# Performance work log

Hardware: AMD Instinct MI355X
Metric: run time of the kernel (lower is better)

The kernel has to match this reference:

```python
import jax, jax.numpy as jnp
import numpy as np

N = 50000      # num_nodes
E = 800000     # num_edges
D = 128        # hidden_dim
POOL_RATIO = 0.5
CROSS_W = 1.0  # cross_weight


def _gcn(x, W, b, src, dst, n):
    """GCNConv: symmetric-normalized aggregation with self-loops. Dropout is identity (eval)."""
    loops = jnp.arange(n)
    s = jnp.concatenate([src, loops])
    d = jnp.concatenate([dst, loops])
    deg = jax.ops.segment_sum(jnp.ones(s.shape, x.dtype), d, num_segments=n)
    inv_sqrt = jax.lax.rsqrt(jnp.maximum(deg, 1.0))  # deg >= 1 due to self-loops
    xw = x @ W                                        # [n, D]
    msg = xw[s] * (inv_sqrt[s] * inv_sqrt[d])[:, None]  # [E+n, D] gather
    return jax.ops.segment_sum(msg, d, num_segments=n) + b


def _prelu(x, a):
    return jnp.where(x >= 0, x, a * x)


def setup_inputs() -> dict:
    key = jax.random.key(0)
    ks = jax.random.split(key, 8)
    glorot = lambda k, sh: jax.random.normal(k, sh, jnp.float32) * np.float32(np.sqrt(2.0 / (sh[0] + sh[1])))
    return {
        "feat": jax.random.normal(ks[0], (N, D), jnp.float32),
        "h_neg": jax.random.normal(ks[1], (N, D), jnp.float32),
        "edge_index": jax.random.randint(ks[2], (2, E), 0, N),
        "Wd": glorot(ks[3], (D, D)),
        "bd": jnp.zeros((D,), jnp.float32),
        "prelu_a": jnp.full((1,), 0.25, jnp.float32),
        "Wbil": glorot(ks[4], (D, D)),
        "bbil": jnp.zeros((1,), jnp.float32),
        "Wg1": glorot(ks[5], (D, D)),
        "bg1": jnp.zeros((D,), jnp.float32),
        "Wg2": glorot(ks[6], (D, D)),
        "bg2": jnp.zeros((D,), jnp.float32),
        "Wg3": glorot(ks[7], (D, D)),
        "bg3": jnp.zeros((D,), jnp.float32),
    }


def reference(feat, h_neg, edge_index, Wd, bd, prelu_a, Wbil, bbil,
              Wg1, bg1, Wg2, bg2, Wg3, bg3):
    src, dst = edge_index[0], edge_index[1]
    # --- IndexSelect: dense layer on pos/neg features ---
    h_pos = _prelu(feat @ Wd + bd, prelu_a)
    h_neg_d = _prelu(h_neg @ Wd + bd, prelu_a)
    embed = _gcn(h_pos, Wg1, bg1, src, dst, N)
    h_center = jax.nn.sigmoid(embed)
    # Discriminator (bilinear) positive scores -> node importance
    score_pos = jnp.einsum('nd,de,ne->n', h_pos, Wbil, h_center) + bbil[0]
    _ = jnp.einsum('nd,de,ne->n', h_neg_d, Wbil, h_center) + bbil[0]  # score_neg (logits branch)
    scores = jax.nn.sigmoid(score_pos)
    order = jnp.argsort(-scores)           # descending
    k = int(POOL_RATIO * N)
    select_idx = order[:k]
    select_scores = scores[order][:k]
    # --- GraphPool (use_gcn=True): down-sample GCN, gather, scale ---
    pooled = _gcn(embed, Wg2, bg2, src, dst, N)[select_idx] * select_scores[:, None]
    # --- GraphUnpool: scatter into zeros, up-sample GCN ---
    fine = jnp.zeros((N, D), feat.dtype).at[select_idx].set(pooled)
    out = _gcn(fine, Wg3, bg3, src, dst, N)
    # --- cross/fuse connection ---
    return out + CROSS_W * embed
```

## Files before the change

kernel.cpp:

```cpp
#include <hip/hip_runtime.h>
#include <hip/hip_bf16.h>

#define NN 50000
#define NE 800000
#define DD 128
#define KSEL 25000
#define NBK 391
#define NBLKA 98

typedef unsigned int uint32;
typedef unsigned short ushort16;

__device__ __forceinline__ float sigmoidf(float x){ return 1.f/(1.f+__expf(-x)); }

__device__ __forceinline__ unsigned short f2b(float f){
  union{float f; unsigned u;} v; v.f=f;
  unsigned r=(v.u + 0x7fffu + ((v.u>>16)&1u))>>16;
  return (unsigned short)r;
}

__device__ __forceinline__ void addbf2(float&lo,float&hi,uint32 u,float w){
  lo+=__uint_as_float(u<<16)*w;
  hi+=__uint_as_float(u&0xffff0000u)*w;
}

__global__ __launch_bounds__(1024) void k_bcount(const int* __restrict__ dst,
    int* __restrict__ btot, int* __restrict__ blkcnt){
  __shared__ int h[NBK];
  int tid=threadIdx.x;
  for(int i=tid;i<NBK;i+=1024) h[i]=0;
  __syncthreads();
  int e0=blockIdx.x*8192;
  #pragma unroll
  for(int t=0;t<8;t++){
    int e=e0+t*1024+tid;
    if(e<NE) atomicAdd(&h[dst[e]>>7],1);
  }
  __syncthreads();
  for(int i=tid;i<NBK;i+=1024){
    int c=h[i];
    blkcnt[blockIdx.x*NBK+i]=c;
    if(c) atomicAdd(&btot[i],c);
  }
}

__global__ __launch_bounds__(512) void k_bscan(const int* __restrict__ btot,
    int* __restrict__ boff, const int* __restrict__ blkcnt, int* __restrict__ blkbase,
    int* __restrict__ row_start){
  __shared__ int sdata[512];
  int tid=threadIdx.x;
  int v=(tid<NBK)?btot[tid]:0;
  sdata[tid]=v; __syncthreads();
  for(int off=1;off<512;off<<=1){
    int y=(tid>=off)?sdata[tid-off]:0;
    __syncthreads();
    sdata[tid]+=y;
    __syncthreads();
  }
  int excl=sdata[tid]-v;
  if(tid<NBK) boff[tid]=excl;
  if(tid==NBK-1){ boff[NBK]=excl+v; row_start[NN]=NE; }
  if(tid<NBK){
    int run=excl;
    for(int b=0;b<NBLKA;b++){
      int c=blkcnt[b*NBK+tid];
      blkbase[b*NBK+tid]=run;
      run+=c;
    }
  }
}

__global__ __launch_bounds__(1024) void k_bscatter(const int* __restrict__ src,
    const int* __restrict__ dst, const int* __restrict__ blkbase, uint32* __restrict__ pairs){
  __shared__ int cur[NBK];
  int tid=threadIdx.x;
  for(int i=tid;i<NBK;i+=1024) cur[i]=blkbase[blockIdx.x*NBK+i];
  __syncthreads();
  int e0=blockIdx.x*8192;
  #pragma unroll
  for(int t=0;t<8;t++){
    int e=e0+t*1024+tid;
    if(e<NE){
      int d=dst[e];
      int p=atomicAdd(&cur[d>>7],1);
      pairs[p]=(unsigned)src[e] | ((unsigned)(d&127)<<17);
    }
  }
}

__global__ __launch_bounds__(256) void k_bfinal(const uint32* __restrict__ pairs,
    const int* __restrict__ boff, int* __restrict__ row_start,
    float* __restrict__ inv_sq, int* __restrict__ csr_src){
  __shared__ int degl[128];
  __shared__ int cur[128];
  __shared__ int ssum[2];
  int b=blockIdx.x, tid=threadIdx.x;
  int lo=boff[b], hi=boff[b+1];
  if(tid<128) degl[tid]=0;
  __syncthreads();
  for(int e=lo+tid;e<hi;e+=256) atomicAdd(&degl[pairs[e]>>17],1);
  __syncthreads();
  int v=0,x=0;
  if(tid<128){
    v=degl[tid]; x=v;
    #pragma unroll
    for(int off=1;off<64;off<<=1){
      int y=__shfl_up(x,off,64);
      if((tid&63)>=off) x+=y;
    }
    if((tid&63)==63) ssum[tid>>6]=x;
  }
  __syncthreads();
  if(tid<128){
    int incl=x+((tid>=64)?ssum[0]:0);
    int node=b*128+tid;
    int excl=lo+incl-v;
    if(node<NN){
      row_start[node]=excl;
      cur[tid]=excl;
      inv_sq[node]=1.f/sqrtf((float)(v+1));
    }
  }
  __syncthreads();
  for(int e=lo+tid;e<hi;e+=256){
    uint32 u=pairs[e];
    int p=atomicAdd(&cur[u>>17],1);
    csr_src[p]=(int)(u&0x1FFFFu);
  }
}

__global__ void k_transpose(const float* __restrict__ W, float* __restrict__ Wt){
  int idx=blockIdx.x*256+threadIdx.x;
  if(idx<DD*DD){
    int k=idx>>7, c=idx&127;
    Wt[idx]=W[c*DD+k];
  }
}

template<int IN_SIG,int ACT,int OUT_BF16,int FUSE_SCORE,int ROWLIST>
__global__ __launch_bounds__(256) void k_gemm96(const float* __restrict__ A,
    const float* __restrict__ W, const float* __restrict__ bias,
    float* __restrict__ outf, ushort16* __restrict__ outb,
    const float* __restrict__ aparam, const float* __restrict__ hp,
    const float* __restrict__ bbil, float* __restrict__ score,
    const int* __restrict__ rlist){
  __shared__ float Al[96][132];
  int tid=threadIdx.x;
  int row0=blockIdx.x*96;
  {
    #pragma unroll
    for(int i=0;i<12;i++){
      int idx=i*256+tid;
      int r=idx>>5, c=(idx&31)*4;
      int gr; bool ok;
      if(ROWLIST){ int ri=row0+r; ok=(ri<KSEL); gr=ok?rlist[ri]:0; }
      else { gr=row0+r; ok=(gr<NN); }
      float4 v=make_float4(0.f,0.f,0.f,0.f);
      if(ok) v=*(const float4*)&A[(size_t)gr*DD+c];
      if(IN_SIG){ v.x=sigmoidf(v.x); v.y=sigmoidf(v.y); v.z=sigmoidf(v.z); v.w=sigmoidf(v.w); }
      *(float4*)&Al[r][c]=v;
    }
  }
  __syncthreads();
  int tx=tid&15, ty=tid>>4;
  float acc[6][8];
  #pragma unroll
  for(int i=0;i<6;i++)
    #pragma unroll
    for(int c=0;c<8;c++) acc[i][c]=0.f;

  for(int k=0;k<DD;k+=4){
    float wv[4][8];
    #pragma unroll
    for(int r=0;r<4;r++){
      float4 lo=*(const float4*)&W[(size_t)(k+r)*DD+tx*8];
      float4 hi=*(const float4*)&W[(size_t)(k+r)*DD+tx*8+4];
      wv[r][0]=lo.x; wv[r][1]=lo.y; wv[r][2]=lo.z; wv[r][3]=lo.w;
      wv[r][4]=hi.x; wv[r][5]=hi.y; wv[r][6]=hi.z; wv[r][7]=hi.w;
    }
    #pragma unroll
    for(int i=0;i<6;i++){
      float4 a=*(const float4*)&Al[ty+16*i][k];
      #pragma unroll
      for(int c=0;c<8;c++)
        acc[i][c]+=a.x*wv[0][c]+a.y*wv[1][c]+a.z*wv[2][c]+a.w*wv[3][c];
    }
  }

  if(FUSE_SCORE){
    float bb=bbil[0];
    #pragma unroll
    for(int i=0;i<6;i++){
      int r=row0+ty+16*i;
      float p=0.f;
      if(r<NN){
        float4 h0=*(const float4*)&hp[(size_t)r*DD+tx*8];
        float4 h1=*(const float4*)&hp[(size_t)r*DD+tx*8+4];
        p=acc[i][0]*h0.x+acc[i][1]*h0.y+acc[i][2]*h0.z+acc[i][3]*h0.w
         +acc[i][4]*h1.x+acc[i][5]*h1.y+acc[i][6]*h1.z+acc[i][7]*h1.w;
      }
      p+=__shfl_xor(p,1,64); p+=__shfl_xor(p,2,64);
      p+=__shfl_xor(p,4,64); p+=__shfl_xor(p,8,64);
      if(tx==0 && r<NN) score[r]=sigmoidf(p+bb);
    }
    return;
  }
  float bl[8]={0,0,0,0,0,0,0,0};
  if(bias){
    float4 b0=*(const float4*)&bias[tx*8];
    float4 b1=*(const float4*)&bias[tx*8+4];
    bl[0]=b0.x; bl[1]=b0.y; bl[2]=b0.z; bl[3]=b0.w;
    bl[4]=b1.x; bl[5]=b1.y; bl[6]=b1.z; bl[7]=b1.w;
  }
  float ap=ACT?aparam[0]:0.f;
  #pragma unroll
  for(int i=0;i<6;i++){
    int ri=row0+ty+16*i;
    int r; bool ok;
    if(ROWLIST){ ok=(ri<KSEL); r=ok?rlist[ri]:0; }
    else { r=ri; ok=(r<NN); }
    if(ok){
      float o[8];
      #pragma unroll
      for(int c=0;c<8;c++){
        float t=acc[i][c]+bl[c];
        if(ACT) t=t>=0.f?t:ap*t;
        o[c]=t;
      }
      if(OUT_BF16){
        uint4 pk;
        pk.x=((uint32)f2b(o[1])<<16)|f2b(o[0]);
        pk.y=((uint32)f2b(o[3])<<16)|f2b(o[2]);
        pk.z=((uint32)f2b(o[5])<<16)|f2b(o[4]);
        pk.w=((uint32)f2b(o[7])<<16)|f2b(o[6]);
        *(uint4*)&outb[(size_t)r*DD+tx*8]=pk;
      } else {
        float4 q0; q0.x=o[0]; q0.y=o[1]; q0.z=o[2]; q0.w=o[3];
        float4 q1; q1.x=o[4]; q1.y=o[5]; q1.z=o[6]; q1.w=o[7];
        *(float4*)&outf[(size_t)r*DD+tx*8]=q0;
        *(float4*)&outf[(size_t)r*DD+tx*8+4]=q1;
      }
    }
  }
}

__global__ __launch_bounds__(256) void k_agg_f32(const float* __restrict__ xw,
    const int* __restrict__ row_start, const int* __restrict__ csr,
    const float* __restrict__ inv, const float* __restrict__ bias,
    float* __restrict__ outp){
  int node=blockIdx.x*4+(threadIdx.x>>6);
  if(node>=NN) return;
  int lane=threadIdx.x&63;
  int g=lane>>5, li=lane&31;
  int rs=row_start[node], re=row_start[node+1];
  float a0=0.f,a1=0.f,a2=0.f,a3=0.f;
  int j=rs;
  for(; j+7<re; j+=8){
    int s0=csr[j+g], s1=csr[j+2+g], s2=csr[j+4+g], s3=csr[j+6+g];
    float w0=inv[s0], w1=inv[s1], w2=inv[s2], w3=inv[s3];
    float4 v0=*(const float4*)&xw[(size_t)s0*DD+li*4];
    float4 v1=*(const float4*)&xw[(size_t)s1*DD+li*4];
    float4 v2=*(const float4*)&xw[(size_t)s2*DD+li*4];
    float4 v3=*(const float4*)&xw[(size_t)s3*DD+li*4];
    a0+=v0.x*w0+v1.x*w1+v2.x*w2+v3.x*w3;
    a1+=v0.y*w0+v1.y*w1+v2.y*w2+v3.y*w3;
    a2+=v0.z*w0+v1.z*w1+v2.z*w2+v3.z*w3;
    a3+=v0.w*w0+v1.w*w1+v2.w*w2+v3.w*w3;
  }
  for(; j+1<re; j+=2){
    int s=csr[j+g];
    float w=inv[s];
    float4 v=*(const float4*)&xw[(size_t)s*DD+li*4];
    a0+=v.x*w; a1+=v.y*w; a2+=v.z*w; a3+=v.w*w;
  }
  if(j<re && g==0){
    int s=csr[j]; float w=inv[s];
    float4 v=*(const float4*)&xw[(size_t)s*DD+li*4];
    a0+=v.x*w; a1+=v.y*w; a2+=v.z*w; a3+=v.w*w;
  }
  if(g==0){
    float wd=inv[node];
    float4 v=*(const float4*)&xw[(size_t)node*DD+li*4];
    a0+=v.x*wd; a1+=v.y*wd; a2+=v.z*wd; a3+=v.w*wd;
  }
  a0+=__shfl_xor(a0,32,64); a1+=__shfl_xor(a1,32,64);
  a2+=__shfl_xor(a2,32,64); a3+=__shfl_xor(a3,32,64);
  if(g==0){
    float wn=inv[node];
    float4 bv=*(const float4*)&bias[li*4];
    float4 o;
    o.x=a0*wn+bv.x; o.y=a1*wn+bv.y; o.z=a2*wn+bv.z; o.w=a3*wn+bv.w;
    *(float4*)&outp[(size_t)node*DD+li*4]=o;
  }
}

template<int MODE>
__global__ __launch_bounds__(256) void k_agg_b16(const uint32* __restrict__ xwb,
    const int* __restrict__ row_start, const int* __restrict__ csr,
    const float* __restrict__ inv, const float* __restrict__ bias,
    float* __restrict__ outp, const float* __restrict__ score,
    const unsigned char* __restrict__ sel, const float* __restrict__ addbuf,
    const int* __restrict__ list){
  int idx4=blockIdx.x*4+(threadIdx.x>>6);
  int node;
  if(MODE==1){ if(idx4>=KSEL) return; node=list[idx4]; }
  else { node=idx4; if(node>=NN) return; }
  int lane=threadIdx.x&63;
  int g=lane>>4, li=lane&15;
  int rs=row_start[node], re=row_start[node+1];
  float a[8];
  #pragma unroll
  for(int c=0;c<8;c++) a[c]=0.f;
  int j=rs;
  for(; j+7<re; j+=8){
    int sA=csr[j+g], sB=csr[j+4+g];
    if(MODE!=2 || sel[sA]){
      float w=inv[sA];
      uint4 u=*(const uint4*)(xwb+(size_t)sA*64+li*4);
      addbf2(a[0],a[1],u.x,w); addbf2(a[2],a[3],u.y,w);
      addbf2(a[4],a[5],u.z,w); addbf2(a[6],a[7],u.w,w);
    }
    if(MODE!=2 || sel[sB]){
      float w=inv[sB];
      uint4 u=*(const uint4*)(xwb+(size_t)sB*64+li*4);
      addbf2(a[0],a[1],u.x,w); addbf2(a[2],a[3],u.y,w);
      addbf2(a[4],a[5],u.z,w); addbf2(a[6],a[7],u.w,w);
    }
  }
  for(; j+3<re; j+=4){
    int s=csr[j+g];
    if(MODE!=2 || sel[s]){
      float w=inv[s];
      uint4 u=*(const uint4*)(xwb+(size_t)s*64+li*4);
      addbf2(a[0],a[1],u.x,w); addbf2(a[2],a[3],u.y,w);
      addbf2(a[4],a[5],u.z,w); addbf2(a[6],a[7],u.w,w);
    }
  }
  int rem=re-j;
  if(g<rem){
    int s=csr[j+g];
    if(MODE!=2 || sel[s]){
      float w=inv[s];
      uint4 u=*(const uint4*)(xwb+(size_t)s*64+li*4);
      addbf2(a[0],a[1],u.x,w); addbf2(a[2],a[3],u.y,w);
      addbf2(a[4],a[5],u.z,w); addbf2(a[6],a[7],u.w,w);
    }
  }
  if(g==0 && (MODE!=2 || sel[node])){
    float wd=inv[node];
    uint4 u=*(const uint4*)(xwb+(size_t)node*64+li*4);
    addbf2(a[0],a[1],u.x,wd); addbf2(a[2],a[3],u.y,wd);
    addbf2(a[4],a[5],u.z,wd); addbf2(a[6],a[7],u.w,wd);
  }
  #pragma unroll
  for(int c=0;c<8;c++){
    a[c]+=__shfl_xor(a[c],16,64);
    a[c]+=__shfl_xor(a[c],32,64);
  }
  if(g<2){
    float wn=inv[node];
    int cb=li*8+g*4;
    float4 bv=*(const float4*)&bias[cb];
    float r0=a[g*4+0]*wn+bv.x, r1=a[g*4+1]*wn+bv.y;
    float r2=a[g*4+2]*wn+bv.z, r3=a[g*4+3]*wn+bv.w;
    if(MODE==1){
      float sc=score[node];
      r0*=sc; r1*=sc; r2*=sc; r3*=sc;
    } else {
      float4 ad=*(const float4*)&addbuf[(size_t)node*DD+cb];
      r0+=ad.x; r1+=ad.y; r2+=ad.z; r3+=ad.w;
    }
    float4 o; o.x=r0; o.y=r1; o.z=r2; o.w=r3;
    *(float4*)&outp[(size_t)node*DD+cb]=o;
  }
}

template<int NB,int PASS>
__global__ __launch_bounds__(256) void k_hist(const float* __restrict__ score,
    int* __restrict__ ghist, const int* __restrict__ ctrl){
  __shared__ int lh[NB];
  int tid=threadIdx.x;
  for(int i=tid;i<NB;i+=256) lh[i]=0;
  __syncthreads();
  int p0=0,p01=0;
  if(PASS==1) p0=ctrl[0];
  if(PASS==2) p01=ctrl[2];
  for(int i=blockIdx.x*256+tid; i<NN; i+=gridDim.x*256){
    unsigned b=__float_as_uint(score[i]);
    if(PASS==0) atomicAdd(&lh[b>>20],1);
    else if(PASS==1){ if((int)(b>>20)==p0) atomicAdd(&lh[(b>>8)&0xFFF],1); }
    else { if((int)(b>>8)==p01) atomicAdd(&lh[b&0xFF],1); }
  }
  __syncthreads();
  for(int i=tid;i<NB;i+=256){ int v=lh[i]; if(v) atomicAdd(&ghist[i],v); }
}

template<int NB,int PASS>
__global__ void k_findb(const int* __restrict__ hist, int* __restrict__ ctrl){
  const int NT=NB/4;
  __shared__ int gsum[NT];
  int t=threadIdx.x;
  int s=hist[t*4]+hist[t*4+1]+hist[t*4+2]+hist[t*4+3];
  int x=s; gsum[t]=x; __syncthreads();
  for(int off=1;off<NT;off<<=1){
    int y=(t+off<NT)?gsum[t+off]:0;
    __syncthreads();
    x+=y; gsum[t]=x; __syncthreads();
  }
  int base;
  if(PASS==0) base=0; else if(PASS==1) base=ctrl[1]; else base=ctrl[3];
  int above=base+((t<NT-1)?gsum[t+1]:0);
  int incl=base+gsum[t];
  if(above<KSEL && incl>=KSEL){
    int c=above, B=0;
    for(int b=3;b>=0;b--){
      int hb=hist[t*4+b];
      if(c+hb>=KSEL){ B=t*4+b; break; }
      c+=hb;
    }
    if(PASS==0){ ctrl[0]=B; ctrl[1]=c; }
    else if(PASS==1){ ctrl[2]=(ctrl[0]<<12)|B; ctrl[3]=c; }
    else { ctrl[4]=(int)((((unsigned)ctrl[2])<<8)|(unsigned)B); ctrl[5]=KSEL-c; }
  }
}

__global__ void k_sel(const float* __restrict__ score, int* __restrict__ ctrl,
                      int* __restrict__ tie_list, unsigned char* __restrict__ sel,
                      int* __restrict__ list){
  int i=blockIdx.x*256+threadIdx.x;
  if(i>=NN) return;
  unsigned b=__float_as_uint(score[i]);
  unsigned thr=(unsigned)ctrl[4];
  if(b>thr){
    sel[i]=1;
    int p=atomicAdd(&ctrl[7],1);
    list[p]=i;
  }
  else if(b==thr){
    sel[i]=0;
    int p=atomicAdd(&ctrl[6],1);
    if(p<4096) tie_list[p]=i;
  } else sel[i]=0;
}

__global__ __launch_bounds__(256) void k_tie(const int* __restrict__ ctrl_c,
    int* __restrict__ ctrl, const int* __restrict__ tie_list,
    unsigned char* __restrict__ sel, int* __restrict__ list){
  int m=ctrl_c[6]; if(m>4096) m=4096;
  int needed=ctrl_c[5];
  for(int t=threadIdx.x; t<m; t+=blockDim.x){
    int idx=tie_list[t];
    int rank=0;
    for(int j=0;j<m;j++) rank+=(tie_list[j]<idx)?1:0;
    if(rank<needed){
      sel[idx]=1;
      int p=atomicAdd(&ctrl[7],1);
      list[p]=idx;
    }
  }
}

extern "C" void kernel_launch(void* const* d_in, const int* in_sizes, int n_in,
                              void* d_out, int out_size, void* d_ws, size_t ws_size,
                              hipStream_t stream){
  const float* feat   =(const float*)d_in[0];
  const int*   ei     =(const int*)  d_in[2];
  const int*   src    = ei;
  const int*   dst    = ei + NE;
  const float* Wd     =(const float*)d_in[3];
  const float* bd     =(const float*)d_in[4];
  const float* prelu_a=(const float*)d_in[5];
  const float* Wbil   =(const float*)d_in[6];
  const float* bbil   =(const float*)d_in[7];
  const float* Wg1    =(const float*)d_in[8];
  const float* bg1    =(const float*)d_in[9];
  const float* Wg2    =(const float*)d_in[10];
  const float* bg2    =(const float*)d_in[11];
  const float* Wg3    =(const float*)d_in[12];
  const float* bg3    =(const float*)d_in[13];
  float* out=(float*)d_out;

  char* p=(char*)d_ws;
  auto alloc=[&](size_t bytes)->void*{ void* r=(void*)p; p+=((bytes+255)/256)*256; return r; };
  float* h_pos   =(float*)alloc((size_t)NN*DD*4);
  float* embed   =(float*)alloc((size_t)NN*DD*4);
  float* xw      =(float*)alloc((size_t)NN*DD*4);
  float* score   =(float*)alloc((size_t)NN*4);
  float* inv_sq  =(float*)alloc((size_t)NN*4);
  float* WbT     =(float*)alloc((size_t)DD*DD*4);
  int*   row_st  =(int*)  alloc((size_t)(NN+1)*4);
  int*   csr_src =(int*)  alloc((size_t)NE*4);
  int*   ctrl    =(int*)  alloc(64);
  int*   hist0   =(int*)  alloc(4096*4);
  int*   hist1   =(int*)  alloc(4096*4);
  int*   hist2   =(int*)  alloc(256*4);
  int*   tie_list=(int*)  alloc(4096*4);
  int*   list    =(int*)  alloc((size_t)KSEL*4);
  unsigned char* sel=(unsigned char*)alloc(NN);
  int*   btot    =(int*)  alloc((size_t)NBK*4);
  int*   boff    =(int*)  alloc((size_t)(NBK+1)*4);
  int*   blkcnt  =(int*)  alloc((size_t)NBLKA*NBK*4);
  int*   blkbase =(int*)  alloc((size_t)NBLKA*NBK*4);
  uint32* pairs  =(uint32*)xw;
  ushort16* xwb  =(ushort16*)xw;
  float* fine = out;

  const int NB=(NN+255)/256;
  const int GB=(NN+95)/96;
  const int GBL=(KSEL+95)/96;
  const int AB=(NN+3)/4;
  const int ABL=(KSEL+3)/4;

  hipMemsetAsync(ctrl, 0, (size_t)((char*)tie_list-(char*)ctrl), stream);
  hipMemsetAsync(btot, 0, (size_t)NBK*4, stream);

  k_bcount  <<<NBLKA,1024,0,stream>>>(dst, btot, blkcnt);
  k_bscan   <<<1,512,0,stream>>>(btot, boff, blkcnt, blkbase, row_st);
  k_bscatter<<<NBLKA,1024,0,stream>>>(src, dst, blkbase, pairs);
  k_bfinal  <<<NBK,256,0,stream>>>(pairs, boff, row_st, inv_sq, csr_src);
  k_transpose<<<64,256,0,stream>>>(Wbil, WbT);

  k_gemm96<0,1,0,0,0><<<GB,256,0,stream>>>(feat, Wd, bd, h_pos, nullptr, prelu_a, nullptr, nullptr, nullptr, nullptr);
  k_gemm96<0,0,0,0,0><<<GB,256,0,stream>>>(h_pos, Wg1, nullptr, xw, nullptr, nullptr, nullptr, nullptr, nullptr, nullptr);
  k_agg_f32<<<AB,256,0,stream>>>(xw, row_st, csr_src, inv_sq, bg1, embed);
  k_gemm96<1,0,0,1,0><<<GB,256,0,stream>>>(embed, WbT, nullptr, nullptr, nullptr, nullptr, h_pos, bbil, score, nullptr);
  k_hist<4096,0><<<64,256,0,stream>>>(score, hist0, ctrl);
  k_findb<4096,0><<<1,1024,0,stream>>>(hist0, ctrl);
  k_hist<4096,1><<<64,256,0,stream>>>(score, hist1, ctrl);
  k_findb<4096,1><<<1,1024,0,stream>>>(hist1, ctrl);
  k_hist<256,2><<<64,256,0,stream>>>(score, hist2, ctrl);
  k_findb<256,2><<<1,64,0,stream>>>(hist2, ctrl);
  k_sel<<<NB,256,0,stream>>>(score, ctrl, tie_list, sel, list);
  k_tie<<<1,256,0,stream>>>(ctrl, ctrl, tie_list, sel, list);
  k_gemm96<0,0,1,0,0><<<GB,256,0,stream>>>(embed, Wg2, nullptr, nullptr, xwb, nullptr, nullptr, nullptr, nullptr, nullptr);
  k_agg_b16<1><<<ABL,256,0,stream>>>((const uint32*)xwb, row_st, csr_src, inv_sq, bg2, fine, score, sel, nullptr, list);
  k_gemm96<0,0,1,0,1><<<GBL,256,0,stream>>>(fine, Wg3, nullptr, nullptr, xwb, nullptr, nullptr, nullptr, nullptr, list);
  k_agg_b16<2><<<AB,256,0,stream>>>((const uint32*)xwb, row_st, csr_src, inv_sq, bg3, out, nullptr, sel, embed, nullptr);
}
```

Measured before the change: 374.4 us.

## Fuse dense and first GCN GEMMs, merge prep kernels, split f32 aggregation by column halves

Measured after the change: 376.4 us. No clear change (+0.5%).

```diff
diff --git a/kernel.cpp b/kernel.cpp
--- a/kernel.cpp
+++ b/kernel.cpp
@@ -7,6 +7,7 @@
 #define KSEL 25000
 #define NBK 391
 #define NBLKA 98
+#define AB 12500
 
 typedef unsigned int uint32;
 typedef unsigned short ushort16;
@@ -22,6 +23,14 @@
 __device__ __forceinline__ void addbf2(float&lo,float&hi,uint32 u,float w){
   lo+=__uint_as_float(u<<16)*w;
   hi+=__uint_as_float(u&0xffff0000u)*w;
+}
+
+__global__ __launch_bounds__(256) void k_prep(const float* __restrict__ W,
+    float* __restrict__ Wt, int* __restrict__ zspan, int* __restrict__ btot){
+  int i=blockIdx.x*256+threadIdx.x;
+  if(i<DD*DD) Wt[i]=W[(i&127)*DD+(i>>7)];
+  if(i<8512) zspan[i]=0;
+  if(i<NBK) btot[i]=0;
 }
 
 __global__ __launch_bounds__(1024) void k_bcount(const int* __restrict__ dst,
@@ -129,11 +138,103 @@
   }
 }
 
-__global__ void k_transpose(const float* __restrict__ W, float* __restrict__ Wt){
-  int idx=blockIdx.x*256+threadIdx.x;
-  if(idx<DD*DD){
-    int k=idx>>7, c=idx&127;
-    Wt[idx]=W[c*DD+k];
+__global__ __launch_bounds__(256) void k_gemm_dual(const float* __restrict__ feat,
+    const float* __restrict__ Wd, const float* __restrict__ bd,
+    const float* __restrict__ aparam, const float* __restrict__ Wg1,
+    float* __restrict__ h_pos, float* __restrict__ xw1){
+  __shared__ float Al[96][132];
+  int tid=threadIdx.x;
+  int row0=blockIdx.x*96;
+  {
+    const float4* A4=(const float4*)(feat+(size_t)row0*DD);
+    #pragma unroll
+    for(int i=0;i<12;i++){
+      int idx=i*256+tid;
+      int r=idx>>5, c=(idx&31)*4;
+      float4 v=make_float4(0.f,0.f,0.f,0.f);
+      if(row0+r<NN) v=A4[idx];
+      *(float4*)&Al[r][c]=v;
+    }
+  }
+  __syncthreads();
+  int tx=tid&15, ty=tid>>4;
+  float acc[6][8];
+  #pragma unroll
+  for(int i=0;i<6;i++)
+    #pragma unroll
+    for(int c=0;c<8;c++) acc[i][c]=0.f;
+  for(int k=0;k<DD;k+=4){
+    float wv[4][8];
+    #pragma unroll
+    for(int r=0;r<4;r++){
+      float4 lo=*(const float4*)&Wd[(size_t)(k+r)*DD+tx*8];
+      float4 hi=*(const float4*)&Wd[(size_t)(k+r)*DD+tx*8+4];
+      wv[r][0]=lo.x; wv[r][1]=lo.y; wv[r][2]=lo.z; wv[r][3]=lo.w;
+      wv[r][4]=hi.x; wv[r][5]=hi.y; wv[r][6]=hi.z; wv[r][7]=hi.w;
+    }
+    #pragma unroll
+    for(int i=0;i<6;i++){
+      float4 a=*(const float4*)&Al[ty+16*i][k];
+      #pragma unroll
+      for(int c=0;c<8;c++)
+        acc[i][c]+=a.x*wv[0][c]+a.y*wv[1][c]+a.z*wv[2][c]+a.w*wv[3][c];
+    }
+  }
+  {
+    float4 b0=*(const float4*)&bd[tx*8];
+    float4 b1=*(const float4*)&bd[tx*8+4];
+    float bl[8]={b0.x,b0.y,b0.z,b0.w,b1.x,b1.y,b1.z,b1.w};
+    float ap=aparam[0];
+    __syncthreads();
+    #pragma unroll
+    for(int i=0;i<6;i++){
+      #pragma unroll
+      for(int c=0;c<8;c++){
+        float t=acc[i][c]+bl[c];
+        acc[i][c]=t>=0.f?t:ap*t;
+      }
+      int r=row0+ty+16*i;
+      float4 q0; q0.x=acc[i][0]; q0.y=acc[i][1]; q0.z=acc[i][2]; q0.w=acc[i][3];
+      float4 q1; q1.x=acc[i][4]; q1.y=acc[i][5]; q1.z=acc[i][6]; q1.w=acc[i][7];
+      if(r<NN){
+        *(float4*)&h_pos[(size_t)r*DD+tx*8]=q0;
+        *(float4*)&h_pos[(size_t)r*DD+tx*8+4]=q1;
+      }
+      *(float4*)&Al[ty+16*i][tx*8]=q0;
+      *(float4*)&Al[ty+16*i][tx*8+4]=q1;
+    }
+  }
+  __syncthreads();
+  #pragma unroll
+  for(int i=0;i<6;i++)
+    #pragma unroll
+    for(int c=0;c<8;c++) acc[i][c]=0.f;
+  for(int k=0;k<DD;k+=4){
+    float wv[4][8];
+    #pragma unroll
+    for(int r=0;r<4;r++){
+      float4 lo=*(const float4*)&Wg1[(size_t)(k+r)*DD+tx*8];
+      float4 hi=*(const float4*)&Wg1[(size_t)(k+r)*DD+tx*8+4];
+      wv[r][0]=lo.x; wv[r][1]=lo.y; wv[r][2]=lo.z; wv[r][3]=lo.w;
+      wv[r][4]=hi.x; wv[r][5]=hi.y; wv[r][6]=hi.z; wv[r][7]=hi.w;
+    }
+    #pragma unroll
+    for(int i=0;i<6;i++){
+      float4 a=*(const float4*)&Al[ty+16*i][k];
+      #pragma unroll
+      for(int c=0;c<8;c++)
+        acc[i][c]+=a.x*wv[0][c]+a.y*wv[1][c]+a.z*wv[2][c]+a.w*wv[3][c];
+    }
+  }
+  #pragma unroll
+  for(int i=0;i<6;i++){
+    int r=row0+ty+16*i;
+    if(r<NN){
+      float4 q0; q0.x=acc[i][0]; q0.y=acc[i][1]; q0.z=acc[i][2]; q0.w=acc[i][3];
+      float4 q1; q1.x=acc[i][4]; q1.y=acc[i][5]; q1.z=acc[i][6]; q1.w=acc[i][7];
+      *(float4*)&xw1[(size_t)r*DD+tx*8]=q0;
+      *(float4*)&xw1[(size_t)r*DD+tx*8+4]=q1;
+    }
   }
 }
 
@@ -244,53 +345,61 @@
   }
 }
 
-__global__ __launch_bounds__(256) void k_agg_f32(const float* __restrict__ xw,
+__global__ __launch_bounds__(256) void k_agg_f32h(const float* __restrict__ xw,
     const int* __restrict__ row_start, const int* __restrict__ csr,
     const float* __restrict__ inv, const float* __restrict__ bias,
     float* __restrict__ outp){
-  int node=blockIdx.x*4+(threadIdx.x>>6);
+  int bid=blockIdx.x;
+  int half=(bid>=AB)?1:0;
+  int node=(bid-half*AB)*4+(threadIdx.x>>6);
   if(node>=NN) return;
   int lane=threadIdx.x&63;
-  int g=lane>>5, li=lane&31;
+  int g=lane>>4, li=lane&15;
+  int colbase=half*64;
+  const float* xwc=xw+colbase;
   int rs=row_start[node], re=row_start[node+1];
   float a0=0.f,a1=0.f,a2=0.f,a3=0.f;
   int j=rs;
-  for(; j+7<re; j+=8){
-    int s0=csr[j+g], s1=csr[j+2+g], s2=csr[j+4+g], s3=csr[j+6+g];
+  for(; j+15<re; j+=16){
+    int s0=csr[j+g], s1=csr[j+4+g], s2=csr[j+8+g], s3=csr[j+12+g];
     float w0=inv[s0], w1=inv[s1], w2=inv[s2], w3=inv[s3];
-    float4 v0=*(const float4*)&xw[(size_t)s0*DD+li*4];
-    float4 v1=*(const float4*)&xw[(size_t)s1*DD+li*4];
-    float4 v2=*(const float4*)&xw[(size_t)s2*DD+li*4];
-    float4 v3=*(const float4*)&xw[(size_t)s3*DD+li*4];
+    float4 v0=*(const float4*)&xwc[(size_t)s0*DD+li*4];
+    float4 v1=*(const float4*)&xwc[(size_t)s1*DD+li*4];
+    float4 v2=*(const float4*)&xwc[(size_t)s2*DD+li*4];
+    float4 v3=*(const float4*)&xwc[(size_t)s3*DD+li*4];
     a0+=v0.x*w0+v1.x*w1+v2.x*w2+v3.x*w3;
     a1+=v0.y*w0+v1.y*w1+v2.y*w2+v3.y*w3;
     a2+=v0.z*w0+v1.z*w1+v2.z*w2+v3.z*w3;
     a3+=v0.w*w0+v1.w*w1+v2.w*w2+v3.w*w3;
   }
-  for(; j+1<re; j+=2){
+  for(; j+3<re; j+=4){
     int s=csr[j+g];
     float w=inv[s];
-    float4 v=*(const float4*)&xw[(size_t)s*DD+li*4];
+    float4 v=*(const float4*)&xwc[(size_t)s*DD+li*4];
     a0+=v.x*w; a1+=v.y*w; a2+=v.z*w; a3+=v.w*w;
   }
-  if(j<re && g==0){
-    int s=csr[j]; float w=inv[s];
-    float4 v=*(const float4*)&xw[(size_t)s*DD+li*4];
+  int rem=re-j;
+  if(g<rem){
+    int s=csr[j+g];
+    float w=inv[s];
+    float4 v=*(const float4*)&xwc[(size_t)s*DD+li*4];
     a0+=v.x*w; a1+=v.y*w; a2+=v.z*w; a3+=v.w*w;
   }
   if(g==0){
     float wd=inv[node];
-    float4 v=*(const float4*)&xw[(size_t)node*DD+li*4];
+    float4 v=*(const float4*)&xwc[(size_t)node*DD+li*4];
     a0+=v.x*wd; a1+=v.y*wd; a2+=v.z*wd; a3+=v.w*wd;
   }
-  a0+=__shfl_xor(a0,32,64); a1+=__shfl_xor(a1,32,64);
-  a2+=__shfl_xor(a2,32,64); a3+=__shfl_xor(a3,32,64);
+  a0+=__shfl_xor(a0,16,64); a0+=__shfl_xor(a0,32,64);
+  a1+=__shfl_xor(a1,16,64); a1+=__shfl_xor(a1,32,64);
+  a2+=__shfl_xor(a2,16,64); a2+=__shfl_xor(a2,32,64);
+  a3+=__shfl_xor(a3,16,64); a3+=__shfl_xor(a3,32,64);
   if(g==0){
     float wn=inv[node];
-    float4 bv=*(const float4*)&bias[li*4];
+    float4 bv=*(const float4*)&bias[colbase+li*4];
     float4 o;
     o.x=a0*wn+bv.x; o.y=a1*wn+bv.y; o.z=a2*wn+bv.z; o.w=a3*wn+bv.w;
-    *(float4*)&outp[(size_t)node*DD+li*4]=o;
+    *(float4*)&outp[(size_t)node*DD+colbase+li*4]=o;
   }
 }
 
@@ -508,21 +617,17 @@
   const int NB=(NN+255)/256;
   const int GB=(NN+95)/96;
   const int GBL=(KSEL+95)/96;
-  const int AB=(NN+3)/4;
   const int ABL=(KSEL+3)/4;
 
-  hipMemsetAsync(ctrl, 0, (size_t)((char*)tie_list-(char*)ctrl), stream);
-  hipMemsetAsync(btot, 0, (size_t)NBK*4, stream);
+  k_prep<<<64,256,0,stream>>>(Wbil, WbT, ctrl, btot);
 
   k_bcount  <<<NBLKA,1024,0,stream>>>(dst, btot, blkcnt);
   k_bscan   <<<1,512,0,stream>>>(btot, boff, blkcnt, blkbase, row_st);
   k_bscatter<<<NBLKA,1024,0,stream>>>(src, dst, blkbase, pairs);
   k_bfinal  <<<NBK,256,0,stream>>>(pairs, boff, row_st, inv_sq, csr_src);
-  k_transpose<<<64,256,0,stream>>>(Wbil, WbT);
-
-  k_gemm96<0,1,0,0,0><<<GB,256,0,stream>>>(feat, Wd, bd, h_pos, nullptr, prelu_a, nullptr, nullptr, nullptr, nullptr);
-  k_gemm96<0,0,0,0,0><<<GB,256,0,stream>>>(h_pos, Wg1, nullptr, xw, nullptr, nullptr, nullptr, nullptr, nullptr, nullptr);
-  k_agg_f32<<<AB,256,0,stream>>>(xw, row_st, csr_src, inv_sq, bg1, embed);
+
+  k_gemm_dual<<<GB,256,0,stream>>>(feat, Wd, bd, prelu_a, Wg1, h_pos, xw);
+  k_agg_f32h<<<2*AB,256,0,stream>>>(xw, row_st, csr_src, inv_sq, bg1, embed);
   k_gemm96<1,0,0,1,0><<<GB,256,0,stream>>>(embed, WbT, nullptr, nullptr, nullptr, nullptr, h_pos, bbil, score, nullptr);
   k_hist<4096,0><<<64,256,0,stream>>>(score, hist0, ctrl);
   k_findb<4096,0><<<1,1024,0,stream>>>(hist0, ctrl);
@@ -535,5 +640,5 @@
   k_gemm96<0,0,1,0,0><<<GB,256,0,stream>>>(embed, Wg2, nullptr, nullptr, xwb, nullptr, nullptr, nullptr, nullptr, nullptr);
   k_agg_b16<1><<<ABL,256,0,stream>>>((const uint32*)xwb, row_st, csr_src, inv_sq, bg2, fine, score, sel, nullptr, list);
   k_gemm96<0,0,1,0,1><<<GBL,256,0,stream>>>(fine, Wg3, nullptr, nullptr, xwb, nullptr, nullptr, nullptr, nullptr, list);
-  k_agg_b16<2><<<AB,256,0,stream>>>((const uint32*)xwb, row_st, csr_src, inv_sq, bg3, out, nullptr, sel, embed, nullptr);
-}
+  k_agg_b16<2><<<2*AB/2,256,0,stream>>>((const uint32*)xwb, row_st, csr_src, inv_sq, bg3, out, nullptr, sel, embed, nullptr);
+}
```
